# Performance work log

Hardware: AMD Instinct MI355X
Metric: run time of the kernel (lower is better)

The kernel has to match this reference:

```python
import jax, jax.numpy as jnp
import numpy as np

EPS = 1e-8

def setup_inputs() -> dict:
    key = jax.random.key(0)
    ks = jax.random.split(key, 12)
    bsz, input_dim, output_dim = 65536, 512, 512
    base_mem_size, category_mem_size, mem_dim, n_cat = 100, 5, 64, 35
    def kaiming(k, shape):
        fan_in = shape[-1]
        bound = np.sqrt(6.0 / fan_in)  # kaiming_uniform with a=sqrt(5) default gain approximated by gain=1 uniform: sqrt(6/fan_in)
        return jax.random.uniform(k, shape, jnp.float32, -bound, bound)
    def linear(kw, kb, out_d, in_d):
        bound = 1.0 / np.sqrt(in_d)
        W = jax.random.uniform(kw, (out_d, in_d), jnp.float32, -bound, bound)
        b = jax.random.uniform(kb, (out_d,), jnp.float32, -bound, bound)
        return W, b
    W_base, b_base = linear(ks[0], ks[1], mem_dim, input_dim)
    W_cat, b_cat = linear(ks[2], ks[3], mem_dim, input_dim)
    W_out, b_out = linear(ks[4], ks[5], output_dim, 2 * mem_dim)
    base_keys = kaiming(ks[6], (base_mem_size, mem_dim))
    base_vals = kaiming(ks[7], (base_mem_size, mem_dim))
    cat_keys = kaiming(ks[8], (n_cat, category_mem_size, mem_dim))
    cat_vals = kaiming(ks[9], (n_cat, category_mem_size, mem_dim))
    query = jax.random.normal(ks[10], (bsz, input_dim), jnp.float32)
    category_idxs = jax.random.randint(ks[11], (bsz,), 0, n_cat)
    return {"query": query, "category_idxs": category_idxs,
            "W_base": W_base, "b_base": b_base, "W_cat": W_cat, "b_cat": b_cat,
            "base_keys": base_keys, "base_vals": base_vals,
            "cat_keys": cat_keys, "cat_vals": cat_vals,
            "W_out": W_out, "b_out": b_out}

def _l2norm(x, axis=-1):
    n = jnp.sqrt(jnp.sum(x * x, axis=axis, keepdims=True))
    return x / jnp.maximum(n, EPS)

def reference(query, category_idxs, W_base, b_base, W_cat, b_cat,
              base_keys, base_vals, cat_keys, cat_vals, W_out, b_out):
    # --- base memory lookup (cosine sim + softmax + weighted sum) ---
    base_query = query @ W_base.T + b_base                      # [b, d]
    base_sims = _l2norm(base_query) @ _l2norm(base_keys).T      # [b, M]
    base_attn = jax.nn.softmax(base_sims, axis=-1)
    base_lookup = base_attn @ base_vals                         # [b, d]
    # --- category memory lookup (gather + dot + softmax + weighted sum) ---
    cat_query = query @ W_cat.T + b_cat                         # [b, d]
    ck = cat_keys[category_idxs]                                # [b, K, d]
    cv = cat_vals[category_idxs]                                # [b, K, d]
    cat_sims = jnp.einsum('bd,bkd->bk', cat_query, ck)          # [b, K]
    cat_attn = jax.nn.softmax(cat_sims, axis=-1)
    cat_lookup = jnp.einsum('bk,bkd->bd', cat_attn, cv)         # [b, d]
    # --- output projection ---
    combined = jnp.concatenate([base_lookup, cat_lookup], axis=1)  # [b, 2d]
    return combined @ W_out.T + b_out                           # [b, out]
```

## Files before the change

kernel.cpp:

```cpp
#include <hip/hip_runtime.h>

typedef _Float16 f16;
typedef _Float16 f16x4 __attribute__((ext_vector_type(4)));
typedef _Float16 f16x8 __attribute__((ext_vector_type(8)));
typedef float    f32x4 __attribute__((ext_vector_type(4)));

#define BATCH 65536
#define INDIM 512
#define MD    64
#define MSZ   100
#define NCAT  35
#define CKSZ  5
#define ODIM  512
#define N1    256
#define K2    128
#define NSLOT (NCAT*CKSZ)
#define RBS   232

static __device__ __forceinline__ f32x4 mfma16(f16x4 a, f16x4 b, f32x4 c) {
  return __builtin_amdgcn_mfma_f32_16x16x16f16(a, b, c, 0, 0, 0);
}

__global__ __launch_bounds__(256) void k_prep(
    const float* __restrict__ Wb, const float* __restrict__ bb,
    const float* __restrict__ Wc, const float* __restrict__ bc,
    const float* __restrict__ keys, const float* __restrict__ bvals,
    const float* __restrict__ cvals, const float* __restrict__ Wo,
    f16* __restrict__ B1, float* __restrict__ bias1,
    f16* __restrict__ B2p, f16* __restrict__ C2cat) {
  int id = blockIdx.x * 256 + threadIdx.x;
  if (id < N1 * INDIM) {
    int k = id & (INDIM - 1);
    int n = id >> 9;
    float v = 0.f;
    if (n < 64) v = Wb[n * INDIM + k];
    else if (n < 128) v = Wc[(n - 64) * INDIM + k];
    else if (n < 128 + MSZ) {
      int m = n - 128;
      float s = 0.f;
      for (int d = 0; d < MD; d++) { float kv = keys[m * MD + d]; s += kv * kv; }
      float dn = fmaxf(sqrtf(s), 1e-8f);
      float a = 0.f;
      for (int d = 0; d < MD; d++) a += Wb[d * INDIM + k] * keys[m * MD + d];
      v = a / dn;
    }
    B1[n * INDIM + k] = (f16)v;
    if (k == 0) {
      float bv = 0.f;
      if (n < 64) bv = bb[n];
      else if (n < 128) bv = bc[n - 64];
      else if (n < 128 + MSZ) {
        int m = n - 128;
        float s = 0.f;
        for (int d = 0; d < MD; d++) { float kv = keys[m * MD + d]; s += kv * kv; }
        float dn = fmaxf(sqrtf(s), 1e-8f);
        float a = 0.f;
        for (int d = 0; d < MD; d++) a += bb[d] * keys[m * MD + d];
        bv = a / dn;
      }
      bias1[n] = bv;
    }
  } else if (id < N1 * INDIM + 16384) {
    int q2 = id - N1 * INDIM;
    int l = q2 & 63, otile = q2 >> 9;
    int o = otile * 16 + (l & 15);
    int kkb = ((q2 >> 6) & 7) * 16 + 4 * (l >> 4);
    float v0 = 0.f, v1 = 0.f, v2 = 0.f, v3 = 0.f;
    if (kkb < MSZ) {
      for (int d = 0; d < MD; d++) {
        float w = Wo[o * 128 + d];
        v0 += bvals[(kkb + 0) * MD + d] * w;
        v1 += bvals[(kkb + 1) * MD + d] * w;
        v2 += bvals[(kkb + 2) * MD + d] * w;
        v3 += bvals[(kkb + 3) * MD + d] * w;
      }
    }
    f16x4 o4; o4[0] = (f16)v0; o4[1] = (f16)v1; o4[2] = (f16)v2; o4[3] = (f16)v3;
    *(f16x4*)(B2p + (size_t)q2 * 4) = o4;
  } else if (id < N1 * INDIM + 16384 + NSLOT * ODIM) {
    int id3 = id - N1 * INDIM - 16384;
    int s = id3 >> 9, o = id3 & 511;
    float a = 0.f;
    for (int d = 0; d < MD; d++) a += cvals[s * MD + d] * Wo[o * 128 + 64 + d];
    C2cat[(size_t)s * ODIM + o] = (f16)a;
  }
}

__global__ __launch_bounds__(512) void k_g1mid(const float* __restrict__ q,
    const f16* __restrict__ B1, const float* __restrict__ bias1,
    const int* __restrict__ cidx, const float* __restrict__ catk,
    f16* __restrict__ A2, float* __restrict__ cwg, int* __restrict__ csg) {
  __shared__ __align__(16) char smem[128 * RBS * 2];
  f16 (*Al)[40] = (f16(*)[40])smem;
  f16 (*Bl)[40] = (f16(*)[40])(smem + 10240);
  f16 (*rb)[RBS] = (f16(*)[RBS])smem;

  const int tid = threadIdx.x;
  const int lane = tid & 63, wid = tid >> 6;
  const int wm = wid & 1, wn = wid >> 1;
  const int row0 = blockIdx.x * 128;
  const int l15 = lane & 15, l4 = lane >> 4;
  f32x4 acc[4][4];
#pragma unroll
  for (int i = 0; i < 4; i++)
#pragma unroll
    for (int j = 0; j < 4; j++) acc[i][j] = (f32x4){0.f, 0.f, 0.f, 0.f};

  const int arow = tid >> 2, aseg = tid & 3;
  const int brow = tid >> 1, bh = tid & 1;

  for (int k0 = 0; k0 < INDIM; k0 += 32) {
    const float* qp = q + (size_t)(row0 + arow) * INDIM + k0 + aseg * 8;
    f32x4 a0 = *(const f32x4*)qp;
    f32x4 a1 = *(const f32x4*)(qp + 4);
    f16x8 av;
#pragma unroll
    for (int i = 0; i < 4; i++) { av[i] = (f16)a0[i]; av[4 + i] = (f16)a1[i]; }
    const f16* bp = B1 + brow * INDIM + k0 + bh * 16;
    f16x8 bv0 = *(const f16x8*)bp;
    f16x8 bv1 = *(const f16x8*)(bp + 8);
    __syncthreads();
    *(f16x8*)&Al[arow][aseg * 8] = av;
    *(f16x8*)&Bl[brow][bh * 16] = bv0;
    *(f16x8*)&Bl[brow][bh * 16 + 8] = bv1;
    __syncthreads();
#pragma unroll
    for (int kk = 0; kk < 2; kk++) {
      const int kc = kk * 16 + 4 * l4;
      f16x4 af[4], bf[4];
#pragma unroll
      for (int mi = 0; mi < 4; mi++) af[mi] = *(const f16x4*)&Al[wm * 64 + mi * 16 + l15][kc];
#pragma unroll
      for (int ni = 0; ni < 4; ni++) bf[ni] = *(const f16x4*)&Bl[wn * 64 + ni * 16 + l15][kc];
#pragma unroll
      for (int mi = 0; mi < 4; mi++)
#pragma unroll
        for (int ni = 0; ni < 4; ni++)
          acc[mi][ni] = mfma16(af[mi], bf[ni], acc[mi][ni]);
    }
  }
  __syncthreads();

#pragma unroll
  for (int ni = 0; ni < 4; ni++) {
    const int col = wn * 64 + ni * 16 + l15;
    const float bs = bias1[col];
    if (col < RBS) {
#pragma unroll
      for (int mi = 0; mi < 4; mi++) {
        const int r = wm * 64 + mi * 16 + 4 * l4;
#pragma unroll
        for (int j = 0; j < 4; j++)
          rb[r + j][col] = (f16)(acc[mi][ni][j] + bs);
      }
    }
  }
  __syncthreads();

  {
    const int row = tid >> 2, s = tid & 3;
    f16x8 v0 = *(const f16x8*)&rb[row][s * 16];
    f16x8 v1 = *(const f16x8*)&rb[row][s * 16 + 8];
    float nb = 0.f;
#pragma unroll
    for (int i = 0; i < 8; i++) { float x = (float)v0[i]; nb += x * x; }
#pragma unroll
    for (int i = 0; i < 8; i++) { float x = (float)v1[i]; nb += x * x; }
    nb += __shfl_xor(nb, 1, 64);
    nb += __shfl_xor(nb, 2, 64);
    const float rinv = 1.f / fmaxf(sqrtf(nb), 1e-8f);

    float sv[25];
#pragma unroll
    for (int i = 0; i < 25; i++)
      sv[i] = (float)rb[row][128 + s * 25 + i] * rinv;
    float mx = sv[0];
#pragma unroll
    for (int i = 1; i < 25; i++) mx = fmaxf(mx, sv[i]);
    mx = fmaxf(mx, __shfl_xor(mx, 1, 64));
    mx = fmaxf(mx, __shfl_xor(mx, 2, 64));
    float es = 0.f;
#pragma unroll
    for (int i = 0; i < 25; i++) { sv[i] = __expf(sv[i] - mx); es += sv[i]; }
    es += __shfl_xor(es, 1, 64);
    es += __shfl_xor(es, 2, 64);
    const float isum = 1.f / es;

    const int ci = cidx[row0 + row];
    const float* kp = catk + (size_t)ci * (CKSZ * MD) + s * 16;
    f16x8 c0 = *(const f16x8*)&rb[row][64 + s * 16];
    f16x8 c1 = *(const f16x8*)&rb[row][64 + s * 16 + 8];
    float cqf[16];
#pragma unroll
    for (int i = 0; i < 8; i++) { cqf[i] = (float)c0[i]; cqf[8 + i] = (float)c1[i]; }
    float t[5];
#pragma unroll
    for (int sl = 0; sl < 5; sl++) {
      f32x4 k0 = *(const f32x4*)(kp + sl * MD);
      f32x4 k1 = *(const f32x4*)(kp + sl * MD + 4);
      f32x4 k2 = *(const f32x4*)(kp + sl * MD + 8);
      f32x4 k3 = *(const f32x4*)(kp + sl * MD + 12);
      float a = 0.f;
#pragma unroll
      for (int i = 0; i < 4; i++) a += cqf[i] * k0[i];
#pragma unroll
      for (int i = 0; i < 4; i++) a += cqf[4 + i] * k1[i];
#pragma unroll
      for (int i = 0; i < 4; i++) a += cqf[8 + i] * k2[i];
#pragma unroll
      for (int i = 0; i < 4; i++) a += cqf[12 + i] * k3[i];
      a += __shfl_xor(a, 1, 64);
      a += __shfl_xor(a, 2, 64);
      t[sl] = a;
    }

#pragma unroll
    for (int i = 0; i < 25; i++)
      rb[row][128 + s * 25 + i] = (f16)(sv[i] * isum);

    if (s == 0) {
      float m5 = fmaxf(fmaxf(fmaxf(t[0], t[1]), fmaxf(t[2], t[3])), t[4]);
      float e0 = __expf(t[0] - m5), e1 = __expf(t[1] - m5), e2 = __expf(t[2] - m5),
            e3 = __expf(t[3] - m5), e4 = __expf(t[4] - m5);
      float ics = 1.f / (e0 + e1 + e2 + e3 + e4);
      float* cwr = cwg + (size_t)(row0 + row) * 5;
      cwr[0] = e0 * ics; cwr[1] = e1 * ics; cwr[2] = e2 * ics;
      cwr[3] = e3 * ics; cwr[4] = e4 * ics;
      csg[row0 + row] = ci * CKSZ;
    }
  }
  __syncthreads();

  {
    const int row = tid >> 2, s = tid & 3;
    f16 tmp[32];
#pragma unroll
    for (int i = 0; i < 32; i++) {
      const int k = s * 32 + i;
      tmp[i] = (k < MSZ) ? rb[row][128 + k] : (f16)0.f;
    }
    f16* dst = A2 + (size_t)(row0 + row) * K2 + s * 32;
#pragma unroll
    for (int i = 0; i < 4; i++)
      *(f16x8*)(dst + i * 8) = *(const f16x8*)&tmp[i * 8];
  }
}

__global__ __launch_bounds__(512) void k_gemm2(const f16* __restrict__ A2,
    const f16* __restrict__ B2p, const float* __restrict__ cwg,
    const int* __restrict__ csg, const f16* __restrict__ C2cat,
    const float* __restrict__ bout, float* __restrict__ out) {
  __shared__ f16 As[128][136];
  __shared__ float cws[128][5];
  __shared__ int csi[128];
  const int tid = threadIdx.x;
  const int lane = tid & 63, wid = tid >> 6;
  const int wm = wid & 1, wn = wid >> 1;
  const int l15 = lane & 15, l4 = lane >> 4;
  const int row0 = blockIdx.x * 128;
  const int col0 = blockIdx.y * 256;

  {
    const int r = tid >> 2, seg = tid & 3;
    const f16* src = A2 + (size_t)(row0 + r) * K2 + seg * 32;
#pragma unroll
    for (int i = 0; i < 4; i++)
      *(f16x8*)&As[r][seg * 32 + i * 8] = *(const f16x8*)(src + i * 8);
  }
  if (tid < 128) {
#pragma unroll
    for (int i = 0; i < 5; i++) cws[tid][i] = cwg[(size_t)(row0 + tid) * 5 + i];
    csi[tid] = csg[row0 + tid];
  }
  __syncthreads();

  f32x4 acc[4][4];
#pragma unroll
  for (int i = 0; i < 4; i++)
#pragma unroll
    for (int j = 0; j < 4; j++) acc[i][j] = (f32x4){0.f, 0.f, 0.f, 0.f};

#pragma unroll
  for (int ks = 0; ks < 8; ks++) {
    f16x4 af[4], bf[4];
#pragma unroll
    for (int mi = 0; mi < 4; mi++)
      af[mi] = *(const f16x4*)&As[wm * 64 + mi * 16 + l15][ks * 16 + 4 * l4];
#pragma unroll
    for (int ni = 0; ni < 4; ni++)
      bf[ni] = *(const f16x4*)(B2p +
        (((size_t)(blockIdx.y * 16 + wn * 4 + ni) * 8 + ks) * 64 + lane) * 4);
#pragma unroll
    for (int mi = 0; mi < 4; mi++)
#pragma unroll
      for (int ni = 0; ni < 4; ni++)
        acc[mi][ni] = mfma16(af[mi], bf[ni], acc[mi][ni]);
  }

  float bs[4];
#pragma unroll
  for (int ni = 0; ni < 4; ni++) bs[ni] = bout[col0 + wn * 64 + ni * 16 + l15];
#pragma unroll
  for (int mi = 0; mi < 4; mi++) {
#pragma unroll
    for (int j = 0; j < 4; j++) {
      const int r = wm * 64 + mi * 16 + 4 * l4 + j;
      const int cb = csi[r];
      const float w0 = cws[r][0], w1 = cws[r][1], w2 = cws[r][2],
                  w3 = cws[r][3], w4 = cws[r][4];
      const f16* cp = C2cat + (size_t)cb * ODIM + col0 + wn * 64 + l15;
#pragma unroll
      for (int ni = 0; ni < 4; ni++) {
        const int col = col0 + wn * 64 + ni * 16 + l15;
        const f16* cpn = cp + ni * 16;
        float v = acc[mi][ni][j] + bs[ni];
        v += w0 * (float)cpn[0]
           + w1 * (float)cpn[ODIM]
           + w2 * (float)cpn[2 * ODIM]
           + w3 * (float)cpn[3 * ODIM]
           + w4 * (float)cpn[4 * ODIM];
        out[(size_t)(row0 + r) * ODIM + col] = v;
      }
    }
  }
}

extern "C" void kernel_launch(void* const* d_in, const int* in_sizes, int n_in,
                              void* d_out, int out_size, void* d_ws, size_t ws_size,
                              hipStream_t stream) {
  const float* query = (const float*)d_in[0];
  const int*   cidx  = (const int*)d_in[1];
  const float* Wb    = (const float*)d_in[2];
  const float* bb    = (const float*)d_in[3];
  const float* Wc    = (const float*)d_in[4];
  const float* bc    = (const float*)d_in[5];
  const float* bkeys = (const float*)d_in[6];
  const float* bvals = (const float*)d_in[7];
  const float* ckeys = (const float*)d_in[8];
  const float* cvals = (const float*)d_in[9];
  const float* Wo    = (const float*)d_in[10];
  const float* bo    = (const float*)d_in[11];
  float* out = (float*)d_out;

  char* ws = (char*)d_ws;
  f16*   A2    = (f16*)(ws);
  float* cwg   = (float*)(ws + 16777216);
  int*   csg   = (int*)(ws + 18087936);
  f16*   B1    = (f16*)(ws + 18350080);
  f16*   B2p   = (f16*)(ws + 18612224);
  f16*   C2cat = (f16*)(ws + 18743296);
  float* bias1 = (float*)(ws + 18922496);

  const int prep_ids = N1 * INDIM + 16384 + NSLOT * ODIM;
  k_prep<<<dim3((prep_ids + 255) / 256), 256, 0, stream>>>(
      Wb, bb, Wc, bc, bkeys, bvals, cvals, Wo, B1, bias1, B2p, C2cat);
  k_g1mid<<<dim3(BATCH / 128), 512, 0, stream>>>(
      query, B1, bias1, cidx, ckeys, A2, cwg, csg);
  k_gemm2<<<dim3(BATCH / 128, 2), 512, 0, stream>>>(A2, B2p, cwg, csg, C2cat, bo, out);
}
```

Measured before the change: 109.1 us.

## Fuse first GEMM, softmax stage and output GEMM into one kernel

Merges the g1mid and gemm2 kernels into a single kernel. The attention weights stay in LDS and feed the second MFMA GEMM directly, with two 256-column passes per block. This removes the global round trip of the 16 MB A2 intermediate (read twice before), the cwg/csg buffers, and one kernel launch. In exchange the grid for the output stage halves, the LDS tile grows, and launch_bounds(512,4) may add register pressure that cuts occupancy for the output-write phase.

```diff
diff --git a/kernel.cpp b/kernel.cpp
--- a/kernel.cpp
+++ b/kernel.cpp
@@ -13,9 +13,8 @@
 #define CKSZ  5
 #define ODIM  512
 #define N1    256
-#define K2    128
 #define NSLOT (NCAT*CKSZ)
-#define RBS   232
+#define RBS   264
 
 static __device__ __forceinline__ f32x4 mfma16(f16x4 a, f16x4 b, f32x4 c) {
   return __builtin_amdgcn_mfma_f32_16x16x16f16(a, b, c, 0, 0, 0);
@@ -86,14 +85,17 @@
   }
 }
 
-__global__ __launch_bounds__(512) void k_g1mid(const float* __restrict__ q,
+__global__ __launch_bounds__(512, 4) void k_all(const float* __restrict__ q,
     const f16* __restrict__ B1, const float* __restrict__ bias1,
     const int* __restrict__ cidx, const float* __restrict__ catk,
-    f16* __restrict__ A2, float* __restrict__ cwg, int* __restrict__ csg) {
+    const f16* __restrict__ B2p, const f16* __restrict__ C2cat,
+    const float* __restrict__ bout, float* __restrict__ out) {
   __shared__ __align__(16) char smem[128 * RBS * 2];
   f16 (*Al)[40] = (f16(*)[40])smem;
   f16 (*Bl)[40] = (f16(*)[40])(smem + 10240);
   f16 (*rb)[RBS] = (f16(*)[RBS])smem;
+  __shared__ float cws[128][5];
+  __shared__ int   csi[128];
 
   const int tid = threadIdx.x;
   const int lane = tid & 63, wid = tid >> 6;
@@ -145,14 +147,12 @@
   for (int ni = 0; ni < 4; ni++) {
     const int col = wn * 64 + ni * 16 + l15;
     const float bs = bias1[col];
-    if (col < RBS) {
-#pragma unroll
-      for (int mi = 0; mi < 4; mi++) {
-        const int r = wm * 64 + mi * 16 + 4 * l4;
-#pragma unroll
-        for (int j = 0; j < 4; j++)
-          rb[r + j][col] = (f16)(acc[mi][ni][j] + bs);
-      }
+#pragma unroll
+    for (int mi = 0; mi < 4; mi++) {
+      const int r = wm * 64 + mi * 16 + 4 * l4;
+#pragma unroll
+      for (int j = 0; j < 4; j++)
+        rb[r + j][col] = (f16)(acc[mi][ni][j] + bs);
     }
   }
   __syncthreads();
@@ -223,103 +223,59 @@
       float e0 = __expf(t[0] - m5), e1 = __expf(t[1] - m5), e2 = __expf(t[2] - m5),
             e3 = __expf(t[3] - m5), e4 = __expf(t[4] - m5);
       float ics = 1.f / (e0 + e1 + e2 + e3 + e4);
-      float* cwr = cwg + (size_t)(row0 + row) * 5;
-      cwr[0] = e0 * ics; cwr[1] = e1 * ics; cwr[2] = e2 * ics;
-      cwr[3] = e3 * ics; cwr[4] = e4 * ics;
-      csg[row0 + row] = ci * CKSZ;
+      cws[row][0] = e0 * ics; cws[row][1] = e1 * ics; cws[row][2] = e2 * ics;
+      cws[row][3] = e3 * ics; cws[row][4] = e4 * ics;
+      csi[row] = ci * CKSZ;
     }
   }
   __syncthreads();
 
-  {
-    const int row = tid >> 2, s = tid & 3;
-    f16 tmp[32];
-#pragma unroll
-    for (int i = 0; i < 32; i++) {
-      const int k = s * 32 + i;
-      tmp[i] = (k < MSZ) ? rb[row][128 + k] : (f16)0.f;
-    }
-    f16* dst = A2 + (size_t)(row0 + row) * K2 + s * 32;
+  for (int cpass = 0; cpass < 2; cpass++) {
+    const int col0 = cpass * 256;
 #pragma unroll
     for (int i = 0; i < 4; i++)
-      *(f16x8*)(dst + i * 8) = *(const f16x8*)&tmp[i * 8];
-  }
-}
-
-__global__ __launch_bounds__(512) void k_gemm2(const f16* __restrict__ A2,
-    const f16* __restrict__ B2p, const float* __restrict__ cwg,
-    const int* __restrict__ csg, const f16* __restrict__ C2cat,
-    const float* __restrict__ bout, float* __restrict__ out) {
-  __shared__ f16 As[128][136];
-  __shared__ float cws[128][5];
-  __shared__ int csi[128];
-  const int tid = threadIdx.x;
-  const int lane = tid & 63, wid = tid >> 6;
-  const int wm = wid & 1, wn = wid >> 1;
-  const int l15 = lane & 15, l4 = lane >> 4;
-  const int row0 = blockIdx.x * 128;
-  const int col0 = blockIdx.y * 256;
-
-  {
-    const int r = tid >> 2, seg = tid & 3;
-    const f16* src = A2 + (size_t)(row0 + r) * K2 + seg * 32;
-#pragma unroll
-    for (int i = 0; i < 4; i++)
-      *(f16x8*)&As[r][seg * 32 + i * 8] = *(const f16x8*)(src + i * 8);
-  }
-  if (tid < 128) {
-#pragma unroll
-    for (int i = 0; i < 5; i++) cws[tid][i] = cwg[(size_t)(row0 + tid) * 5 + i];
-    csi[tid] = csg[row0 + tid];
-  }
-  __syncthreads();
-
-  f32x4 acc[4][4];
-#pragma unroll
-  for (int i = 0; i < 4; i++)
-#pragma unroll
-    for (int j = 0; j < 4; j++) acc[i][j] = (f32x4){0.f, 0.f, 0.f, 0.f};
-
-#pragma unroll
-  for (int ks = 0; ks < 8; ks++) {
-    f16x4 af[4], bf[4];
-#pragma unroll
-    for (int mi = 0; mi < 4; mi++)
-      af[mi] = *(const f16x4*)&As[wm * 64 + mi * 16 + l15][ks * 16 + 4 * l4];
-#pragma unroll
-    for (int ni = 0; ni < 4; ni++)
-      bf[ni] = *(const f16x4*)(B2p +
-        (((size_t)(blockIdx.y * 16 + wn * 4 + ni) * 8 + ks) * 64 + lane) * 4);
-#pragma unroll
-    for (int mi = 0; mi < 4; mi++)
+#pragma unroll
+      for (int j = 0; j < 4; j++) acc[i][j] = (f32x4){0.f, 0.f, 0.f, 0.f};
+#pragma unroll
+    for (int ks = 0; ks < 8; ks++) {
+      f16x4 af[4], bf[4];
+#pragma unroll
+      for (int mi = 0; mi < 4; mi++)
+        af[mi] = *(const f16x4*)&rb[wm * 64 + mi * 16 + l15][128 + ks * 16 + 4 * l4];
 #pragma unroll
       for (int ni = 0; ni < 4; ni++)
-        acc[mi][ni] = mfma16(af[mi], bf[ni], acc[mi][ni]);
-  }
-
-  float bs[4];
-#pragma unroll
-  for (int ni = 0; ni < 4; ni++) bs[ni] = bout[col0 + wn * 64 + ni * 16 + l15];
-#pragma unroll
-  for (int mi = 0; mi < 4; mi++) {
-#pragma unroll
-    for (int j = 0; j < 4; j++) {
-      const int r = wm * 64 + mi * 16 + 4 * l4 + j;
-      const int cb = csi[r];
-      const float w0 = cws[r][0], w1 = cws[r][1], w2 = cws[r][2],
-                  w3 = cws[r][3], w4 = cws[r][4];
-      const f16* cp = C2cat + (size_t)cb * ODIM + col0 + wn * 64 + l15;
-#pragma unroll
-      for (int ni = 0; ni < 4; ni++) {
-        const int col = col0 + wn * 64 + ni * 16 + l15;
-        const f16* cpn = cp + ni * 16;
-        float v = acc[mi][ni][j] + bs[ni];
-        v += w0 * (float)cpn[0]
-           + w1 * (float)cpn[ODIM]
-           + w2 * (float)cpn[2 * ODIM]
-           + w3 * (float)cpn[3 * ODIM]
-           + w4 * (float)cpn[4 * ODIM];
-        out[(size_t)(row0 + r) * ODIM + col] = v;
+        bf[ni] = *(const f16x4*)(B2p +
+          (((size_t)(cpass * 16 + wn * 4 + ni) * 8 + ks) * 64 + lane) * 4);
+#pragma unroll
+      for (int mi = 0; mi < 4; mi++)
+#pragma unroll
+        for (int ni = 0; ni < 4; ni++)
+          acc[mi][ni] = mfma16(af[mi], bf[ni], acc[mi][ni]);
+    }
+    float bs[4];
+#pragma unroll
+    for (int ni = 0; ni < 4; ni++) bs[ni] = bout[col0 + wn * 64 + ni * 16 + l15];
+#pragma unroll
+    for (int mi = 0; mi < 4; mi++) {
+#pragma unroll
+      for (int j = 0; j < 4; j++) {
+        const int r = wm * 64 + mi * 16 + 4 * l4 + j;
+        const int cb = csi[r];
+        const float w0 = cws[r][0], w1 = cws[r][1], w2 = cws[r][2],
+                    w3 = cws[r][3], w4 = cws[r][4];
+        const f16* cp = C2cat + (size_t)cb * ODIM + col0 + wn * 64 + l15;
+#pragma unroll
+        for (int ni = 0; ni < 4; ni++) {
+          const int col = col0 + wn * 64 + ni * 16 + l15;
+          const f16* cpn = cp + ni * 16;
+          float v = acc[mi][ni][j] + bs[ni];
+          v += w0 * (float)cpn[0]
+             + w1 * (float)cpn[ODIM]
+             + w2 * (float)cpn[2 * ODIM]
+             + w3 * (float)cpn[3 * ODIM]
+             + w4 * (float)cpn[4 * ODIM];
+          out[(size_t)(row0 + r) * ODIM + col] = v;
+        }
       }
     }
   }
@@ -343,18 +299,14 @@
   float* out = (float*)d_out;
 
   char* ws = (char*)d_ws;
-  f16*   A2    = (f16*)(ws);
-  float* cwg   = (float*)(ws + 16777216);
-  int*   csg   = (int*)(ws + 18087936);
-  f16*   B1    = (f16*)(ws + 18350080);
-  f16*   B2p   = (f16*)(ws + 18612224);
-  f16*   C2cat = (f16*)(ws + 18743296);
-  float* bias1 = (float*)(ws + 18922496);
+  f16*   B1    = (f16*)(ws);
+  f16*   B2p   = (f16*)(ws + 262144);
+  f16*   C2cat = (f16*)(ws + 262144 + 131072);
+  float* bias1 = (float*)(ws + 262144 + 131072 + 179200);
 
   const int prep_ids = N1 * INDIM + 16384 + NSLOT * ODIM;
   k_prep<<<dim3((prep_ids + 255) / 256), 256, 0, stream>>>(
       Wb, bb, Wc, bc, bkeys, bvals, cvals, Wo, B1, bias1, B2p, C2cat);
-  k_g1mid<<<dim3(BATCH / 128), 512, 0, stream>>>(
-      query, B1, bias1, cidx, ckeys, A2, cwg, csg);
-  k_gemm2<<<dim3(BATCH / 128, 2), 512, 0, stream>>>(A2, B2p, cwg, csg, C2cat, bo, out);
+  k_all<<<dim3(BATCH / 128), 512, 0, stream>>>(
+      query, B1, bias1, cidx, ckeys, B2p, C2cat, bo, out);
 }
```

After: 243.0 us. 123% more time.
